# Optimization experiments

Measured on AMD Instinct MI355X. Metric: run time of the kernel, lower is better.

Reference implementation:

```python
import jax, jax.numpy as jnp
import numpy as np
import math

N, DIM = 131072, 128
NUM_CODEBOOKS, CODEBOOK_SIZE = 4, 2048
COMMIT_COST = 0.25


def setup_inputs() -> dict:
    key = jax.random.key(0)
    k1, k2 = jax.random.split(key)
    z_e = jax.random.normal(k1, (N, DIM), dtype=jnp.float32)
    codebooks = jax.random.normal(k2, (NUM_CODEBOOKS, CODEBOOK_SIZE, DIM), dtype=jnp.float32) / math.sqrt(DIM)
    return {"z_e": z_e, "codebooks": codebooks}


def _rvq(z_e, codebooks):
    # Sequential residual quantization stages via scan over codebooks.
    def stage(residual, codebook):
        x_norm = jnp.sum(residual * residual, axis=1, keepdims=True)
        c_norm = jnp.sum(codebook * codebook, axis=1)[None, :]
        d = x_norm - 2.0 * (residual @ codebook.T) + c_norm
        idx = jnp.argmin(d, axis=1)            # [N]
        q = codebook[idx]                      # [N, dim]
        return residual - q, (q, idx)

    _, (qs, idxs) = jax.lax.scan(stage, z_e, codebooks)
    quantized_sum = jnp.sum(qs, axis=0)        # [N, dim]
    codes = idxs.T                             # [N, num_codebooks]
    return quantized_sum, codes


def reference(z_e, codebooks):
    quantized_sum, codes = _rvq(z_e, codebooks)
    sg = jax.lax.stop_gradient
    codebook_loss = jnp.mean((sg(quantized_sum) - z_e) ** 2)
    commit_loss = jnp.mean((quantized_sum - sg(z_e)) ** 2)
    loss = codebook_loss + COMMIT_COST * commit_loss
    # straight-through estimator
    z_q = z_e + sg(quantized_sum - z_e)
    return (z_q, codes, loss)
```

## Files before the change

### kernel.cpp

```cpp
#include <hip/hip_runtime.h>

typedef float v16f __attribute__((ext_vector_type(16)));
typedef _Float16 v8h __attribute__((ext_vector_type(8)));

#define NROWS 131072
#define DIM 128
#define NCB 4
#define CBS 2048
#define ZQ_SIZE ((size_t)NROWS * DIM)
#define CODES_SIZE ((size_t)NROWS * NCB)
#define CHUNK_BYTES 16384
#define CBQ_TOTAL ((size_t)NCB * 64 * CHUNK_BYTES)
#define INV4096 2.44140625e-4f

#define MFMA16(a, b, c) __builtin_amdgcn_mfma_f32_32x32x16_f16((a), (b), (c), 0, 0, 0)

__global__ void prep_cb(const float* __restrict__ cb, _Float16* __restrict__ cbq) {
    const int g = blockIdx.x * 256 + threadIdx.x;
    const int c   = g & 7;
    const int col = (g >> 3) & 31;
    const int q   = (g >> 8) & 63;
    const int s   = g >> 14;
    const float* src = cb + (size_t)(s * CBS + q * 32 + col) * DIM + 16 * c;
    _Float16* base = cbq + (size_t)(s * 64 + q) * 8192;
#pragma unroll
    for (int hh = 0; hh < 2; ++hh) {
        v8h p0, p1;
#pragma unroll
        for (int j = 0; j < 8; ++j) {
            const float v = src[8 * hh + j];
            const _Float16 h0 = (_Float16)v;
            const float t = v - (float)h0;
            p0[j] = h0;
            p1[j] = (_Float16)(t * 4096.0f);
        }
        *reinterpret_cast<v8h*>(base + (size_t)c * 512 + (hh * 32 + col) * 8) = p0;
        *reinterpret_cast<v8h*>(base + (size_t)(8 + c) * 512 + (hh * 32 + col) * 8) = p1;
    }
}

__global__ void prep_cn(const float* __restrict__ cb, float* __restrict__ cn) {
    const int g = blockIdx.x * 256 + threadIdx.x;
    const float* src = cb + (size_t)g * DIM;
    float acc = 0.0f;
    for (int i = 0; i < 32; ++i) {
        const float4 v = *reinterpret_cast<const float4*>(src + 4 * i);
        acc = fmaf(v.x, v.x, acc); acc = fmaf(v.y, v.y, acc);
        acc = fmaf(v.z, v.z, acc); acc = fmaf(v.w, v.w, acc);
    }
    cn[g] = acc;
}

__global__ __launch_bounds__(256, 2)
void rvq_main(const float* __restrict__ ze, const float* __restrict__ cbf,
              const _Float16* __restrict__ cbq, const float* __restrict__ cn,
              float* __restrict__ out)
{
    __shared__ __align__(16) char BB[2][CHUNK_BYTES];
    __shared__ float XN[4][32];
    __shared__ int   BIs[4][32];

    const int tid  = threadIdx.x;
    const int wid  = tid >> 6;
    const int lane = tid & 63;
    const int col  = lane & 31;
    const int h    = lane >> 5;
    const int rowbase = blockIdx.x * 128 + wid * 32;
    const int myrow   = rowbase + col;

    float res[8][8];
#pragma unroll
    for (int c = 0; c < 8; ++c) {
#pragma unroll
        for (int w2 = 0; w2 < 2; ++w2) {
            const float4 v = *reinterpret_cast<const float4*>(
                ze + (size_t)myrow * DIM + 16 * c + 8 * h + 4 * w2);
            res[c][4 * w2 + 0] = v.x; res[c][4 * w2 + 1] = v.y;
            res[c][4 * w2 + 2] = v.z; res[c][4 * w2 + 3] = v.w;
        }
    }

    for (int s = 0; s < NCB; ++s) {
        v8h A0[8], A1[8];
        float pc[8];
#pragma unroll
        for (int c = 0; c < 8; ++c) {
            float p[8];
#pragma unroll
            for (int j = 0; j < 8; ++j) {
                const float v = res[c][j];
                p[j] = v * v;
                const _Float16 h0 = (_Float16)v;
                const float t = v - (float)h0;
                A0[c][j] = h0;
                A1[c][j] = (_Float16)(t * 4096.0f);
            }
            pc[c] = ((p[0] + p[1]) + (p[2] + p[3])) + ((p[4] + p[5]) + (p[6] + p[7]));
        }
        float xnp = ((pc[0] + pc[1]) + (pc[2] + pc[3])) + ((pc[4] + pc[5]) + (pc[6] + pc[7]));
        const float xn_own = xnp + __shfl_xor(xnp, 32);
        if (h == 0) XN[wid][col] = xn_own;
        __syncthreads();
        float xns[16];
#pragma unroll
        for (int r = 0; r < 16; ++r) xns[r] = XN[wid][(r & 3) + 8 * (r >> 2) + 4 * h];

        {
            const char* g0 = (const char*)cbq + (size_t)(s * 64) * CHUNK_BYTES;
#pragma unroll
            for (int i = 0; i < 4; ++i) {
                const int blk = i * 4 + wid;
                __builtin_amdgcn_global_load_lds(
                    (const __attribute__((address_space(1))) void*)(g0 + blk * 1024 + lane * 16),
                    (__attribute__((address_space(3))) void*)(&BB[0][blk * 1024]),
                    16, 0, 0);
            }
        }
        __syncthreads();

        float bestd[16]; int besti[16];
#pragma unroll
        for (int r = 0; r < 16; ++r) { bestd[r] = INFINITY; besti[r] = 0; }

#pragma unroll 1
        for (int q = 0; q < 64; ++q) {
            const int cur = q & 1;
            if (q < 63) {
                const char* gq = (const char*)cbq + (size_t)(s * 64 + q + 1) * CHUNK_BYTES;
#pragma unroll
                for (int i = 0; i < 4; ++i) {
                    const int blk = i * 4 + wid;
                    __builtin_amdgcn_global_load_lds(
                        (const __attribute__((address_space(1))) void*)(gq + blk * 1024 + lane * 16),
                        (__attribute__((address_space(3))) void*)(&BB[cur ^ 1][blk * 1024]),
                        16, 0, 0);
                }
            }
            const float cnv = cn[s * CBS + q * 32 + col];
            const char* bb = &BB[cur][0];
            v16f aM, aC;
            {
                const v8h b0 = *reinterpret_cast<const v8h*>(bb + lane * 16);
                const v8h b1 = *reinterpret_cast<const v8h*>(bb + 8 * 1024 + lane * 16);
                const v16f Z = {0.f,0.f,0.f,0.f,0.f,0.f,0.f,0.f,0.f,0.f,0.f,0.f,0.f,0.f,0.f,0.f};
                aM = MFMA16(A0[0], b0, Z);
                aC = MFMA16(A1[0], b0, Z);
                aC = MFMA16(A0[0], b1, aC);
            }
#pragma unroll
            for (int c = 1; c < 8; ++c) {
                const v8h b0 = *reinterpret_cast<const v8h*>(bb + (size_t)c * 1024 + lane * 16);
                const v8h b1 = *reinterpret_cast<const v8h*>(bb + (size_t)(8 + c) * 1024 + lane * 16);
                aM = MFMA16(A0[c], b0, aM);
                aC = MFMA16(A1[c], b0, aC);
                aC = MFMA16(A0[c], b1, aC);
            }
            const int code = q * 32 + col;
#pragma unroll
            for (int r = 0; r < 16; ++r) {
                const float dotf = fmaf(aC[r], INV4096, aM[r]);
                const float d = fmaf(-2.0f, dotf, xns[r]) + cnv;
                if (d < bestd[r]) { bestd[r] = d; besti[r] = code; }
            }
            __syncthreads();
        }

#pragma unroll
        for (int r = 0; r < 16; ++r) {
            float d = bestd[r]; int bi = besti[r];
#pragma unroll
            for (int m = 1; m <= 16; m <<= 1) {
                const float od = __shfl_xor(d, m);
                const int   oi = __shfl_xor(bi, m);
                const bool take = (od < d) || ((od == d) && (oi < bi));
                d  = take ? od : d;
                bi = take ? oi : bi;
            }
            bestd[r] = d; besti[r] = bi;
        }

        if (col == 0) {
#pragma unroll
            for (int r = 0; r < 16; ++r) {
                const int row16 = (r & 3) + 8 * (r >> 2) + 4 * h;
                BIs[wid][row16] = besti[r];
                out[ZQ_SIZE + (size_t)(rowbase + row16) * NCB + s] = (float)besti[r];
            }
        }
        __syncthreads();

        const int mybest = BIs[wid][col];
        const float* qrow = cbf + ((size_t)(s * CBS) + mybest) * DIM + 8 * h;
#pragma unroll
        for (int c = 0; c < 8; ++c) {
#pragma unroll
            for (int w2 = 0; w2 < 2; ++w2) {
                const float4 v = *reinterpret_cast<const float4*>(qrow + 16 * c + 4 * w2);
                res[c][4 * w2 + 0] -= v.x; res[c][4 * w2 + 1] -= v.y;
                res[c][4 * w2 + 2] -= v.z; res[c][4 * w2 + 3] -= v.w;
            }
        }
    }

    float lsum = 0.0f;
#pragma unroll
    for (int c = 0; c < 8; ++c) {
#pragma unroll
        for (int w2 = 0; w2 < 2; ++w2) {
            const float4 z = *reinterpret_cast<const float4*>(
                ze + (size_t)myrow * DIM + 16 * c + 8 * h + 4 * w2);
            const float r0 = res[c][4 * w2 + 0], r1 = res[c][4 * w2 + 1];
            const float r2 = res[c][4 * w2 + 2], r3 = res[c][4 * w2 + 3];
            float4 o;
            o.x = z.x - r0; o.y = z.y - r1; o.z = z.z - r2; o.w = z.w - r3;
            *reinterpret_cast<float4*>(out + (size_t)myrow * DIM + 16 * c + 8 * h + 4 * w2) = o;
            lsum = fmaf(r0, r0, lsum); lsum = fmaf(r1, r1, lsum);
            lsum = fmaf(r2, r2, lsum); lsum = fmaf(r3, r3, lsum);
        }
    }
#pragma unroll
    for (int m = 1; m < 64; m <<= 1) lsum += __shfl_xor(lsum, m);
    if (lane == 0)
        atomicAdd(out + ZQ_SIZE + CODES_SIZE, lsum * (1.25f / 16777216.0f));
}

extern "C" void kernel_launch(void* const* d_in, const int* in_sizes, int n_in,
                              void* d_out, int out_size, void* d_ws, size_t ws_size,
                              hipStream_t stream)
{
    const float* ze  = (const float*)d_in[0];
    const float* cbf = (const float*)d_in[1];
    float* out = (float*)d_out;

    _Float16* cbq = (_Float16*)d_ws;
    float* cnall = (float*)((char*)d_ws + CBQ_TOTAL);

    hipMemsetAsync(out + ZQ_SIZE + CODES_SIZE, 0, sizeof(float), stream);

    prep_cb<<<256, 256, 0, stream>>>(cbf, cbq);
    prep_cn<<<32, 256, 0, stream>>>(cbf, cnall);
    rvq_main<<<NROWS / 128, 256, 0, stream>>>(ze, cbf, cbq, cnall, out);
}
```

Baseline: 857.6 us.

## Recompute residual from history to cut registers, triple-buffer codebook chunks

Stops holding the 64-float residual in registers across stages. Each stage instead rebuilds it from z_e and the codebook rows selected so far. The argmin index is packed as 8-bit chunk ids, norm broadcast uses shuffles instead of LDS, and occupancy is raised to 3 blocks per CU. Codebook chunks are now triple-buffered with explicit vmcnt-based barriers so two chunks are in flight at once. The cost is extra global and cache reloads of z_e and codebook rows, and correctness depends on the hand-written waitcnt barriers.

```diff
diff --git a/kernel.cpp b/kernel.cpp
--- a/kernel.cpp
+++ b/kernel.cpp
@@ -51,14 +51,29 @@
     cn[g] = acc;
 }
 
-__global__ __launch_bounds__(256, 2)
+#define BAR_N4 do { \
+    __builtin_amdgcn_sched_barrier(0); \
+    asm volatile("s_waitcnt vmcnt(4) lgkmcnt(0)" ::: "memory"); \
+    __builtin_amdgcn_s_barrier(); \
+    asm volatile("" ::: "memory"); \
+    __builtin_amdgcn_sched_barrier(0); \
+} while (0)
+
+#define BAR_N0 do { \
+    __builtin_amdgcn_sched_barrier(0); \
+    asm volatile("s_waitcnt vmcnt(0) lgkmcnt(0)" ::: "memory"); \
+    __builtin_amdgcn_s_barrier(); \
+    asm volatile("" ::: "memory"); \
+    __builtin_amdgcn_sched_barrier(0); \
+} while (0)
+
+__global__ __launch_bounds__(256, 3)
 void rvq_main(const float* __restrict__ ze, const float* __restrict__ cbf,
               const _Float16* __restrict__ cbq, const float* __restrict__ cn,
               float* __restrict__ out)
 {
-    __shared__ __align__(16) char BB[2][CHUNK_BYTES];
-    __shared__ float XN[4][32];
-    __shared__ int   BIs[4][32];
+    __shared__ __align__(16) char BB[3][CHUNK_BYTES];
+    __shared__ int BIs[4][32];
 
     const int tid  = threadIdx.x;
     const int wid  = tid >> 6;
@@ -68,27 +83,35 @@
     const int rowbase = blockIdx.x * 128 + wid * 32;
     const int myrow   = rowbase + col;
 
-    float res[8][8];
-#pragma unroll
-    for (int c = 0; c < 8; ++c) {
-#pragma unroll
-        for (int w2 = 0; w2 < 2; ++w2) {
-            const float4 v = *reinterpret_cast<const float4*>(
-                ze + (size_t)myrow * DIM + 16 * c + 8 * h + 4 * w2);
-            res[c][4 * w2 + 0] = v.x; res[c][4 * w2 + 1] = v.y;
-            res[c][4 * w2 + 2] = v.z; res[c][4 * w2 + 3] = v.w;
-        }
-    }
-
+    const float* zrow = ze + (size_t)myrow * DIM + 8 * h;
+    int hist0 = 0, hist1 = 0, hist2 = 0, hist3 = 0;
+
+#pragma unroll
     for (int s = 0; s < NCB; ++s) {
         v8h A0[8], A1[8];
         float pc[8];
 #pragma unroll
         for (int c = 0; c < 8; ++c) {
+            float r8[8];
+            {
+                const float4 v0 = *reinterpret_cast<const float4*>(zrow + 16 * c);
+                const float4 v1 = *reinterpret_cast<const float4*>(zrow + 16 * c + 4);
+                r8[0] = v0.x; r8[1] = v0.y; r8[2] = v0.z; r8[3] = v0.w;
+                r8[4] = v1.x; r8[5] = v1.y; r8[6] = v1.z; r8[7] = v1.w;
+            }
+#pragma unroll
+            for (int t = 0; t < s; ++t) {
+                const int ht = (t == 0) ? hist0 : (t == 1) ? hist1 : (t == 2) ? hist2 : hist3;
+                const float* qrow = cbf + ((size_t)(t * CBS) + ht) * DIM + 16 * c + 8 * h;
+                const float4 q0 = *reinterpret_cast<const float4*>(qrow);
+                const float4 q1 = *reinterpret_cast<const float4*>(qrow + 4);
+                r8[0] -= q0.x; r8[1] -= q0.y; r8[2] -= q0.z; r8[3] -= q0.w;
+                r8[4] -= q1.x; r8[5] -= q1.y; r8[6] -= q1.z; r8[7] -= q1.w;
+            }
             float p[8];
 #pragma unroll
             for (int j = 0; j < 8; ++j) {
-                const float v = res[c][j];
+                const float v = r8[j];
                 p[j] = v * v;
                 const _Float16 h0 = (_Float16)v;
                 const float t = v - (float)h0;
@@ -97,46 +120,48 @@
             }
             pc[c] = ((p[0] + p[1]) + (p[2] + p[3])) + ((p[4] + p[5]) + (p[6] + p[7]));
         }
-        float xnp = ((pc[0] + pc[1]) + (pc[2] + pc[3])) + ((pc[4] + pc[5]) + (pc[6] + pc[7]));
+        const float xnp = ((pc[0] + pc[1]) + (pc[2] + pc[3])) + ((pc[4] + pc[5]) + (pc[6] + pc[7]));
         const float xn_own = xnp + __shfl_xor(xnp, 32);
-        if (h == 0) XN[wid][col] = xn_own;
-        __syncthreads();
         float xns[16];
 #pragma unroll
-        for (int r = 0; r < 16; ++r) xns[r] = XN[wid][(r & 3) + 8 * (r >> 2) + 4 * h];
-
-        {
-            const char* g0 = (const char*)cbq + (size_t)(s * 64) * CHUNK_BYTES;
+        for (int r = 0; r < 16; ++r)
+            xns[r] = __shfl(xn_own, (r & 3) + 8 * (r >> 2) + 4 * h);
+
+        const char* cbq_s = (const char*)cbq + (size_t)(s * 64) * CHUNK_BYTES;
+
+#pragma unroll
+        for (int qq = 0; qq < 2; ++qq) {
+            const char* gsrc = cbq_s + (size_t)qq * CHUNK_BYTES;
 #pragma unroll
             for (int i = 0; i < 4; ++i) {
                 const int blk = i * 4 + wid;
                 __builtin_amdgcn_global_load_lds(
-                    (const __attribute__((address_space(1))) void*)(g0 + blk * 1024 + lane * 16),
-                    (__attribute__((address_space(3))) void*)(&BB[0][blk * 1024]),
-                    16, 0, 0);
-            }
-        }
-        __syncthreads();
-
-        float bestd[16]; int besti[16];
-#pragma unroll
-        for (int r = 0; r < 16; ++r) { bestd[r] = INFINITY; besti[r] = 0; }
-
+                    (const __attribute__((address_space(1))) void*)(gsrc + blk * 1024 + lane * 16),
+                    (__attribute__((address_space(3))) void*)(&BB[qq][blk * 1024]), 16, 0, 0);
+            }
+        }
+        BAR_N4;
+
+        float bestd[16];
+        unsigned bq[4] = {0u, 0u, 0u, 0u};
+#pragma unroll
+        for (int r = 0; r < 16; ++r) bestd[r] = INFINITY;
+
+        int cur = 0;
 #pragma unroll 1
         for (int q = 0; q < 64; ++q) {
-            const int cur = q & 1;
-            if (q < 63) {
-                const char* gq = (const char*)cbq + (size_t)(s * 64 + q + 1) * CHUNK_BYTES;
+            const float cnv = cn[s * CBS + q * 32 + col];
+            if (q < 62) {
+                int pre = cur - 1; if (pre < 0) pre = 2;
+                const char* gsrc = cbq_s + (size_t)(q + 2) * CHUNK_BYTES;
 #pragma unroll
                 for (int i = 0; i < 4; ++i) {
                     const int blk = i * 4 + wid;
                     __builtin_amdgcn_global_load_lds(
-                        (const __attribute__((address_space(1))) void*)(gq + blk * 1024 + lane * 16),
-                        (__attribute__((address_space(3))) void*)(&BB[cur ^ 1][blk * 1024]),
-                        16, 0, 0);
+                        (const __attribute__((address_space(1))) void*)(gsrc + blk * 1024 + lane * 16),
+                        (__attribute__((address_space(3))) void*)(&BB[pre][blk * 1024]), 16, 0, 0);
                 }
             }
-            const float cnv = cn[s * CBS + q * 32 + col];
             const char* bb = &BB[cur][0];
             v16f aM, aC;
             {
@@ -155,16 +180,24 @@
                 aC = MFMA16(A1[c], b0, aC);
                 aC = MFMA16(A0[c], b1, aC);
             }
-            const int code = q * 32 + col;
 #pragma unroll
             for (int r = 0; r < 16; ++r) {
                 const float dotf = fmaf(aC[r], INV4096, aM[r]);
                 const float d = fmaf(-2.0f, dotf, xns[r]) + cnv;
-                if (d < bestd[r]) { bestd[r] = d; besti[r] = code; }
-            }
-            __syncthreads();
-        }
-
+                const bool take = d < bestd[r];
+                bestd[r] = take ? d : bestd[r];
+                const int w = r >> 2, sh = (r & 3) * 8;
+                const unsigned nb = (bq[w] & ~(255u << sh)) | ((unsigned)q << sh);
+                bq[w] = take ? nb : bq[w];
+            }
+            if (q < 62) { BAR_N4; } else { BAR_N0; }
+            cur = (cur == 2) ? 0 : cur + 1;
+        }
+
+        int besti[16];
+#pragma unroll
+        for (int r = 0; r < 16; ++r)
+            besti[r] = (int)((bq[r >> 2] >> ((r & 3) * 8)) & 255u) * 32 + col;
 #pragma unroll
         for (int r = 0; r < 16; ++r) {
             float d = bestd[r]; int bi = besti[r];
@@ -187,36 +220,43 @@
                 out[ZQ_SIZE + (size_t)(rowbase + row16) * NCB + s] = (float)besti[r];
             }
         }
-        __syncthreads();
-
+        asm volatile("s_waitcnt lgkmcnt(0)" ::: "memory");
         const int mybest = BIs[wid][col];
-        const float* qrow = cbf + ((size_t)(s * CBS) + mybest) * DIM + 8 * h;
-#pragma unroll
-        for (int c = 0; c < 8; ++c) {
-#pragma unroll
-            for (int w2 = 0; w2 < 2; ++w2) {
-                const float4 v = *reinterpret_cast<const float4*>(qrow + 16 * c + 4 * w2);
-                res[c][4 * w2 + 0] -= v.x; res[c][4 * w2 + 1] -= v.y;
-                res[c][4 * w2 + 2] -= v.z; res[c][4 * w2 + 3] -= v.w;
-            }
-        }
+        if (s == 0) hist0 = mybest;
+        else if (s == 1) hist1 = mybest;
+        else if (s == 2) hist2 = mybest;
+        else hist3 = mybest;
     }
 
     float lsum = 0.0f;
 #pragma unroll
     for (int c = 0; c < 8; ++c) {
-#pragma unroll
-        for (int w2 = 0; w2 < 2; ++w2) {
-            const float4 z = *reinterpret_cast<const float4*>(
-                ze + (size_t)myrow * DIM + 16 * c + 8 * h + 4 * w2);
-            const float r0 = res[c][4 * w2 + 0], r1 = res[c][4 * w2 + 1];
-            const float r2 = res[c][4 * w2 + 2], r3 = res[c][4 * w2 + 3];
-            float4 o;
-            o.x = z.x - r0; o.y = z.y - r1; o.z = z.z - r2; o.w = z.w - r3;
-            *reinterpret_cast<float4*>(out + (size_t)myrow * DIM + 16 * c + 8 * h + 4 * w2) = o;
-            lsum = fmaf(r0, r0, lsum); lsum = fmaf(r1, r1, lsum);
-            lsum = fmaf(r2, r2, lsum); lsum = fmaf(r3, r3, lsum);
-        }
+        float z8[8], r8[8];
+        {
+            const float4 v0 = *reinterpret_cast<const float4*>(zrow + 16 * c);
+            const float4 v1 = *reinterpret_cast<const float4*>(zrow + 16 * c + 4);
+            z8[0] = v0.x; z8[1] = v0.y; z8[2] = v0.z; z8[3] = v0.w;
+            z8[4] = v1.x; z8[5] = v1.y; z8[6] = v1.z; z8[7] = v1.w;
+        }
+#pragma unroll
+        for (int j = 0; j < 8; ++j) r8[j] = z8[j];
+#pragma unroll
+        for (int t = 0; t < 4; ++t) {
+            const int ht = (t == 0) ? hist0 : (t == 1) ? hist1 : (t == 2) ? hist2 : hist3;
+            const float* qrow = cbf + ((size_t)(t * CBS) + ht) * DIM + 16 * c + 8 * h;
+            const float4 q0 = *reinterpret_cast<const float4*>(qrow);
+            const float4 q1 = *reinterpret_cast<const float4*>(qrow + 4);
+            r8[0] -= q0.x; r8[1] -= q0.y; r8[2] -= q0.z; r8[3] -= q0.w;
+            r8[4] -= q1.x; r8[5] -= q1.y; r8[6] -= q1.z; r8[7] -= q1.w;
+        }
+        float4 o0, o1;
+        o0.x = z8[0] - r8[0]; o0.y = z8[1] - r8[1]; o0.z = z8[2] - r8[2]; o0.w = z8[3] - r8[3];
+        o1.x = z8[4] - r8[4]; o1.y = z8[5] - r8[5]; o1.z = z8[6] - r8[6]; o1.w = z8[7] - r8[7];
+        float* orow = out + (size_t)myrow * DIM + 16 * c + 8 * h;
+        *reinterpret_cast<float4*>(orow) = o0;
+        *reinterpret_cast<float4*>(orow + 4) = o1;
+#pragma unroll
+        for (int j = 0; j < 8; ++j) lsum = fmaf(r8[j], r8[j], lsum);
     }
 #pragma unroll
     for (int m = 1; m < 64; m <<= 1) lsum += __shfl_xor(lsum, m);
```

New measurement: 1.007 ms. 1.17x slower.

## Drop fp32 residual registers via fp16 triple split, raise occupancy to three blocks

Applied to the files above, without the earlier changes.

The fp32 residual array (64 registers per thread) is removed. The residual is instead stored as three fp16 pieces: two kept in registers as MFMA operands and the third spilled to scratch space in the output buffer. It is rebuilt from those pieces at each stage, which frees registers so launch bounds can rise to three blocks per CU. The change also replaces the LDS row-norm exchange and one barrier with wave shuffles, adds s_setprio around the MFMA block, and makes the argmin update branchless. The costs are extra global traffic for the scratch piece, the reconstruction arithmetic, and a slight change in residual precision.

```diff
diff --git a/kernel.cpp b/kernel.cpp
--- a/kernel.cpp
+++ b/kernel.cpp
@@ -51,14 +51,22 @@
     cn[g] = acc;
 }
 
-__global__ __launch_bounds__(256, 2)
+__device__ __forceinline__ void split3(float v, _Float16* h0, _Float16* h1, _Float16* h2) {
+    const _Float16 a = (_Float16)v;
+    const float t1 = v - (float)a;
+    const float s1 = t1 * 4096.0f;
+    const _Float16 b = (_Float16)s1;
+    const float s2 = (s1 - (float)b) * 4096.0f;
+    *h0 = a; *h1 = b; *h2 = (_Float16)s2;
+}
+
+__global__ __launch_bounds__(256, 3)
 void rvq_main(const float* __restrict__ ze, const float* __restrict__ cbf,
               const _Float16* __restrict__ cbq, const float* __restrict__ cn,
               float* __restrict__ out)
 {
     __shared__ __align__(16) char BB[2][CHUNK_BYTES];
-    __shared__ float XN[4][32];
-    __shared__ int   BIs[4][32];
+    __shared__ int BIs[4][32];
 
     const int tid  = threadIdx.x;
     const int wid  = tid >> 6;
@@ -68,53 +76,71 @@
     const int rowbase = blockIdx.x * 128 + wid * 32;
     const int myrow   = rowbase + col;
 
-    float res[8][8];
-#pragma unroll
-    for (int c = 0; c < 8; ++c) {
-#pragma unroll
-        for (int w2 = 0; w2 < 2; ++w2) {
-            const float4 v = *reinterpret_cast<const float4*>(
-                ze + (size_t)myrow * DIM + 16 * c + 8 * h + 4 * w2);
-            res[c][4 * w2 + 0] = v.x; res[c][4 * w2 + 1] = v.y;
-            res[c][4 * w2 + 2] = v.z; res[c][4 * w2 + 3] = v.w;
-        }
-    }
+    const float* zrow = ze + (size_t)myrow * DIM + 8 * h;
+    _Float16* a2 = (_Float16*)out + (size_t)blockIdx.x * 32768;
+
+    v8h A0[8], A1[8];
+    int mylast = 0;
 
     for (int s = 0; s < NCB; ++s) {
-        v8h A0[8], A1[8];
         float pc[8];
-#pragma unroll
-        for (int c = 0; c < 8; ++c) {
-            float p[8];
-#pragma unroll
-            for (int j = 0; j < 8; ++j) {
-                const float v = res[c][j];
-                p[j] = v * v;
-                const _Float16 h0 = (_Float16)v;
-                const float t = v - (float)h0;
-                A0[c][j] = h0;
-                A1[c][j] = (_Float16)(t * 4096.0f);
-            }
-            pc[c] = ((p[0] + p[1]) + (p[2] + p[3])) + ((p[4] + p[5]) + (p[6] + p[7]));
-        }
-        float xnp = ((pc[0] + pc[1]) + (pc[2] + pc[3])) + ((pc[4] + pc[5]) + (pc[6] + pc[7]));
+        if (s == 0) {
+#pragma unroll
+            for (int c = 0; c < 8; ++c) {
+                const float4 v0 = *reinterpret_cast<const float4*>(zrow + 16 * c);
+                const float4 v1 = *reinterpret_cast<const float4*>(zrow + 16 * c + 4);
+                float v[8] = {v0.x, v0.y, v0.z, v0.w, v1.x, v1.y, v1.z, v1.w};
+                v8h a2v;
+                float p[8];
+#pragma unroll
+                for (int j = 0; j < 8; ++j) {
+                    p[j] = v[j] * v[j];
+                    _Float16 x0, x1, x2;
+                    split3(v[j], &x0, &x1, &x2);
+                    A0[c][j] = x0; A1[c][j] = x1; a2v[j] = x2;
+                }
+                *reinterpret_cast<v8h*>(a2 + ((size_t)c * 256 + tid) * 8) = a2v;
+                pc[c] = ((p[0] + p[1]) + (p[2] + p[3])) + ((p[4] + p[5]) + (p[6] + p[7]));
+            }
+        } else {
+            const float* qrow = cbf + ((size_t)((s - 1) * CBS) + mylast) * DIM + 8 * h;
+#pragma unroll
+            for (int c = 0; c < 8; ++c) {
+                const v8h a2v_old = *reinterpret_cast<const v8h*>(a2 + ((size_t)c * 256 + tid) * 8);
+                const float4 q0 = *reinterpret_cast<const float4*>(qrow + 16 * c);
+                const float4 q1 = *reinterpret_cast<const float4*>(qrow + 16 * c + 4);
+                const float qv[8] = {q0.x, q0.y, q0.z, q0.w, q1.x, q1.y, q1.z, q1.w};
+                v8h a2v;
+                float p[8];
+#pragma unroll
+                for (int j = 0; j < 8; ++j) {
+                    const float vr = fmaf((float)a2v_old[j], 0x1p-24f,
+                                     fmaf((float)A1[c][j], 0x1p-12f, (float)A0[c][j]));
+                    const float v = vr - qv[j];
+                    p[j] = v * v;
+                    _Float16 x0, x1, x2;
+                    split3(v, &x0, &x1, &x2);
+                    A0[c][j] = x0; A1[c][j] = x1; a2v[j] = x2;
+                }
+                *reinterpret_cast<v8h*>(a2 + ((size_t)c * 256 + tid) * 8) = a2v;
+                pc[c] = ((p[0] + p[1]) + (p[2] + p[3])) + ((p[4] + p[5]) + (p[6] + p[7]));
+            }
+        }
+        const float xnp = ((pc[0] + pc[1]) + (pc[2] + pc[3])) + ((pc[4] + pc[5]) + (pc[6] + pc[7]));
         const float xn_own = xnp + __shfl_xor(xnp, 32);
-        if (h == 0) XN[wid][col] = xn_own;
-        __syncthreads();
         float xns[16];
 #pragma unroll
-        for (int r = 0; r < 16; ++r) xns[r] = XN[wid][(r & 3) + 8 * (r >> 2) + 4 * h];
-
-        {
-            const char* g0 = (const char*)cbq + (size_t)(s * 64) * CHUNK_BYTES;
-#pragma unroll
-            for (int i = 0; i < 4; ++i) {
-                const int blk = i * 4 + wid;
-                __builtin_amdgcn_global_load_lds(
-                    (const __attribute__((address_space(1))) void*)(g0 + blk * 1024 + lane * 16),
-                    (__attribute__((address_space(3))) void*)(&BB[0][blk * 1024]),
-                    16, 0, 0);
-            }
+        for (int r = 0; r < 16; ++r)
+            xns[r] = __shfl(xn_own, (r & 3) + 8 * (r >> 2) + 4 * h);
+
+        const char* cbq_s = (const char*)cbq + (size_t)(s * 64) * CHUNK_BYTES;
+
+#pragma unroll
+        for (int i = 0; i < 4; ++i) {
+            const int blk = i * 4 + wid;
+            __builtin_amdgcn_global_load_lds(
+                (const __attribute__((address_space(1))) void*)(cbq_s + blk * 1024 + lane * 16),
+                (__attribute__((address_space(3))) void*)(&BB[0][blk * 1024]), 16, 0, 0);
         }
         __syncthreads();
 
@@ -125,20 +151,20 @@
 #pragma unroll 1
         for (int q = 0; q < 64; ++q) {
             const int cur = q & 1;
+            const float cnv = cn[s * CBS + q * 32 + col];
             if (q < 63) {
-                const char* gq = (const char*)cbq + (size_t)(s * 64 + q + 1) * CHUNK_BYTES;
+                const char* gq = cbq_s + (size_t)(q + 1) * CHUNK_BYTES;
 #pragma unroll
                 for (int i = 0; i < 4; ++i) {
                     const int blk = i * 4 + wid;
                     __builtin_amdgcn_global_load_lds(
                         (const __attribute__((address_space(1))) void*)(gq + blk * 1024 + lane * 16),
-                        (__attribute__((address_space(3))) void*)(&BB[cur ^ 1][blk * 1024]),
-                        16, 0, 0);
+                        (__attribute__((address_space(3))) void*)(&BB[cur ^ 1][blk * 1024]), 16, 0, 0);
                 }
             }
-            const float cnv = cn[s * CBS + q * 32 + col];
             const char* bb = &BB[cur][0];
             v16f aM, aC;
+            __builtin_amdgcn_s_setprio(1);
             {
                 const v8h b0 = *reinterpret_cast<const v8h*>(bb + lane * 16);
                 const v8h b1 = *reinterpret_cast<const v8h*>(bb + 8 * 1024 + lane * 16);
@@ -155,12 +181,15 @@
                 aC = MFMA16(A1[c], b0, aC);
                 aC = MFMA16(A0[c], b1, aC);
             }
-            const int code = q * 32 + col;
+            __builtin_amdgcn_s_setprio(0);
+            const int code = (q << 5) | col;
 #pragma unroll
             for (int r = 0; r < 16; ++r) {
                 const float dotf = fmaf(aC[r], INV4096, aM[r]);
                 const float d = fmaf(-2.0f, dotf, xns[r]) + cnv;
-                if (d < bestd[r]) { bestd[r] = d; besti[r] = code; }
+                const bool take = d < bestd[r];
+                bestd[r] = take ? d : bestd[r];
+                besti[r] = take ? code : besti[r];
             }
             __syncthreads();
         }
@@ -188,35 +217,39 @@
             }
         }
         __syncthreads();
-
-        const int mybest = BIs[wid][col];
-        const float* qrow = cbf + ((size_t)(s * CBS) + mybest) * DIM + 8 * h;
-#pragma unroll
-        for (int c = 0; c < 8; ++c) {
-#pragma unroll
-            for (int w2 = 0; w2 < 2; ++w2) {
-                const float4 v = *reinterpret_cast<const float4*>(qrow + 16 * c + 4 * w2);
-                res[c][4 * w2 + 0] -= v.x; res[c][4 * w2 + 1] -= v.y;
-                res[c][4 * w2 + 2] -= v.z; res[c][4 * w2 + 3] -= v.w;
-            }
-        }
-    }
-
+        mylast = BIs[wid][col];
+    }
+
+    v8h a2r[8];
+#pragma unroll
+    for (int c = 0; c < 8; ++c)
+        a2r[c] = *reinterpret_cast<const v8h*>(a2 + ((size_t)c * 256 + tid) * 8);
+    __syncthreads();
+
+    const float* qrow = cbf + ((size_t)(3 * CBS) + mylast) * DIM + 8 * h;
     float lsum = 0.0f;
 #pragma unroll
     for (int c = 0; c < 8; ++c) {
-#pragma unroll
-        for (int w2 = 0; w2 < 2; ++w2) {
-            const float4 z = *reinterpret_cast<const float4*>(
-                ze + (size_t)myrow * DIM + 16 * c + 8 * h + 4 * w2);
-            const float r0 = res[c][4 * w2 + 0], r1 = res[c][4 * w2 + 1];
-            const float r2 = res[c][4 * w2 + 2], r3 = res[c][4 * w2 + 3];
-            float4 o;
-            o.x = z.x - r0; o.y = z.y - r1; o.z = z.z - r2; o.w = z.w - r3;
-            *reinterpret_cast<float4*>(out + (size_t)myrow * DIM + 16 * c + 8 * h + 4 * w2) = o;
-            lsum = fmaf(r0, r0, lsum); lsum = fmaf(r1, r1, lsum);
-            lsum = fmaf(r2, r2, lsum); lsum = fmaf(r3, r3, lsum);
-        }
+        const float4 q0 = *reinterpret_cast<const float4*>(qrow + 16 * c);
+        const float4 q1 = *reinterpret_cast<const float4*>(qrow + 16 * c + 4);
+        const float4 z0 = *reinterpret_cast<const float4*>(zrow + 16 * c);
+        const float4 z1 = *reinterpret_cast<const float4*>(zrow + 16 * c + 4);
+        const float qv[8] = {q0.x, q0.y, q0.z, q0.w, q1.x, q1.y, q1.z, q1.w};
+        const float zv[8] = {z0.x, z0.y, z0.z, z0.w, z1.x, z1.y, z1.z, z1.w};
+        float o[8];
+#pragma unroll
+        for (int j = 0; j < 8; ++j) {
+            const float vr = fmaf((float)a2r[c][j], 0x1p-24f,
+                             fmaf((float)A1[c][j], 0x1p-12f, (float)A0[c][j]));
+            const float v = vr - qv[j];
+            o[j] = zv[j] - v;
+            lsum = fmaf(v, v, lsum);
+        }
+        float4 o0 = {o[0], o[1], o[2], o[3]};
+        float4 o1 = {o[4], o[5], o[6], o[7]};
+        float* orow = out + (size_t)myrow * DIM + 16 * c + 8 * h;
+        *reinterpret_cast<float4*>(orow) = o0;
+        *reinterpret_cast<float4*>(orow + 4) = o1;
     }
 #pragma unroll
     for (int m = 1; m < 64; m <<= 1) lsum += __shfl_xor(lsum, m);
@@ -235,7 +268,7 @@
     _Float16* cbq = (_Float16*)d_ws;
     float* cnall = (float*)((char*)d_ws + CBQ_TOTAL);
 
-    hipMemsetAsync(out + ZQ_SIZE + CODES_SIZE, 0, sizeof(float), stream);
+    (void)hipMemsetAsync(out + ZQ_SIZE + CODES_SIZE, 0, sizeof(float), stream);
 
     prep_cb<<<256, 256, 0, stream>>>(cbf, cbq);
     prep_cn<<<32, 256, 0, stream>>>(cbf, cnall);
```

Measured after the change: 960.9 us. +12.0%, slower.

## Process two codebook chunks per barrier and pack best indices into bytes

Applied to the files above, without the earlier changes.

The main loop now loads 32KB periods (two 32-code chunks) per double-buffer step, which halves the number of block-wide barriers per stage. The first period's load is issued before the residual fp16 split so it overlaps that work. The row norm is broadcast with shuffles instead of going through shared memory. Best-code indices are stored as 8-bit chunk ids packed four per register to save registers, and s_setprio raises wave priority around the MFMA block. The cost is doubled LDS usage (64KB per block), which may limit the two-blocks-per-CU occupancy target.

```diff
diff --git a/kernel.cpp b/kernel.cpp
--- a/kernel.cpp
+++ b/kernel.cpp
@@ -1,6 +1,7 @@
 #include <hip/hip_runtime.h>
 
 typedef float v16f __attribute__((ext_vector_type(16)));
+typedef float v4f __attribute__((ext_vector_type(4)));
 typedef _Float16 v8h __attribute__((ext_vector_type(8)));
 
 #define NROWS 131072
@@ -10,6 +11,7 @@
 #define ZQ_SIZE ((size_t)NROWS * DIM)
 #define CODES_SIZE ((size_t)NROWS * NCB)
 #define CHUNK_BYTES 16384
+#define PERIOD_BYTES 32768
 #define CBQ_TOTAL ((size_t)NCB * 64 * CHUNK_BYTES)
 #define INV4096 2.44140625e-4f
 
@@ -44,7 +46,7 @@
     const float* src = cb + (size_t)g * DIM;
     float acc = 0.0f;
     for (int i = 0; i < 32; ++i) {
-        const float4 v = *reinterpret_cast<const float4*>(src + 4 * i);
+        const v4f v = *reinterpret_cast<const v4f*>(src + 4 * i);
         acc = fmaf(v.x, v.x, acc); acc = fmaf(v.y, v.y, acc);
         acc = fmaf(v.z, v.z, acc); acc = fmaf(v.w, v.w, acc);
     }
@@ -56,9 +58,8 @@
               const _Float16* __restrict__ cbq, const float* __restrict__ cn,
               float* __restrict__ out)
 {
-    __shared__ __align__(16) char BB[2][CHUNK_BYTES];
-    __shared__ float XN[4][32];
-    __shared__ int   BIs[4][32];
+    __shared__ __align__(16) char BB[2][PERIOD_BYTES];
+    __shared__ int BIs[4][32];
 
     const int tid  = threadIdx.x;
     const int wid  = tid >> 6;
@@ -68,19 +69,31 @@
     const int rowbase = blockIdx.x * 128 + wid * 32;
     const int myrow   = rowbase + col;
 
+    const float* zrow = ze + (size_t)myrow * DIM + 8 * h;
+
     float res[8][8];
 #pragma unroll
     for (int c = 0; c < 8; ++c) {
 #pragma unroll
         for (int w2 = 0; w2 < 2; ++w2) {
-            const float4 v = *reinterpret_cast<const float4*>(
-                ze + (size_t)myrow * DIM + 16 * c + 8 * h + 4 * w2);
+            const v4f v = *reinterpret_cast<const v4f*>(zrow + 16 * c + 4 * w2);
             res[c][4 * w2 + 0] = v.x; res[c][4 * w2 + 1] = v.y;
             res[c][4 * w2 + 2] = v.z; res[c][4 * w2 + 3] = v.w;
         }
     }
 
+#pragma unroll 1
     for (int s = 0; s < NCB; ++s) {
+        const char* cbq_s = (const char*)cbq + (size_t)(s * 64) * CHUNK_BYTES;
+
+#pragma unroll
+        for (int u = 0; u < 8; ++u) {
+            const int off = (u * 4 + wid) * 1024 + lane * 16;
+            __builtin_amdgcn_global_load_lds(
+                (const __attribute__((address_space(1))) void*)(cbq_s + off),
+                (__attribute__((address_space(3))) void*)(&BB[0][off]), 16, 0, 0);
+        }
+
         v8h A0[8], A1[8];
         float pc[8];
 #pragma unroll
@@ -97,77 +110,77 @@
             }
             pc[c] = ((p[0] + p[1]) + (p[2] + p[3])) + ((p[4] + p[5]) + (p[6] + p[7]));
         }
-        float xnp = ((pc[0] + pc[1]) + (pc[2] + pc[3])) + ((pc[4] + pc[5]) + (pc[6] + pc[7]));
+        const float xnp = ((pc[0] + pc[1]) + (pc[2] + pc[3])) + ((pc[4] + pc[5]) + (pc[6] + pc[7]));
         const float xn_own = xnp + __shfl_xor(xnp, 32);
-        if (h == 0) XN[wid][col] = xn_own;
+        float xns[16];
+#pragma unroll
+        for (int r = 0; r < 16; ++r)
+            xns[r] = __shfl(xn_own, (r & 3) + 8 * (r >> 2) + 4 * h);
+
+        float bestd[16];
+        unsigned bq[4] = {0u, 0u, 0u, 0u};
+#pragma unroll
+        for (int r = 0; r < 16; ++r) bestd[r] = INFINITY;
+
         __syncthreads();
-        float xns[16];
-#pragma unroll
-        for (int r = 0; r < 16; ++r) xns[r] = XN[wid][(r & 3) + 8 * (r >> 2) + 4 * h];
-
-        {
-            const char* g0 = (const char*)cbq + (size_t)(s * 64) * CHUNK_BYTES;
-#pragma unroll
-            for (int i = 0; i < 4; ++i) {
-                const int blk = i * 4 + wid;
-                __builtin_amdgcn_global_load_lds(
-                    (const __attribute__((address_space(1))) void*)(g0 + blk * 1024 + lane * 16),
-                    (__attribute__((address_space(3))) void*)(&BB[0][blk * 1024]),
-                    16, 0, 0);
-            }
-        }
-        __syncthreads();
-
-        float bestd[16]; int besti[16];
-#pragma unroll
-        for (int r = 0; r < 16; ++r) { bestd[r] = INFINITY; besti[r] = 0; }
 
 #pragma unroll 1
-        for (int q = 0; q < 64; ++q) {
-            const int cur = q & 1;
-            if (q < 63) {
-                const char* gq = (const char*)cbq + (size_t)(s * 64 + q + 1) * CHUNK_BYTES;
-#pragma unroll
-                for (int i = 0; i < 4; ++i) {
-                    const int blk = i * 4 + wid;
+        for (int p = 0; p < 32; ++p) {
+            const int cur = p & 1;
+            const float cnv0 = cn[s * CBS + (2 * p) * 32 + col];
+            const float cnv1 = cn[s * CBS + (2 * p + 1) * 32 + col];
+            if (p < 31) {
+                const char* gp = cbq_s + (size_t)(p + 1) * PERIOD_BYTES;
+#pragma unroll
+                for (int u = 0; u < 8; ++u) {
+                    const int off = (u * 4 + wid) * 1024 + lane * 16;
                     __builtin_amdgcn_global_load_lds(
-                        (const __attribute__((address_space(1))) void*)(gq + blk * 1024 + lane * 16),
-                        (__attribute__((address_space(3))) void*)(&BB[cur ^ 1][blk * 1024]),
-                        16, 0, 0);
-                }
-            }
-            const float cnv = cn[s * CBS + q * 32 + col];
-            const char* bb = &BB[cur][0];
-            v16f aM, aC;
-            {
-                const v8h b0 = *reinterpret_cast<const v8h*>(bb + lane * 16);
-                const v8h b1 = *reinterpret_cast<const v8h*>(bb + 8 * 1024 + lane * 16);
-                const v16f Z = {0.f,0.f,0.f,0.f,0.f,0.f,0.f,0.f,0.f,0.f,0.f,0.f,0.f,0.f,0.f,0.f};
-                aM = MFMA16(A0[0], b0, Z);
-                aC = MFMA16(A1[0], b0, Z);
-                aC = MFMA16(A0[0], b1, aC);
-            }
-#pragma unroll
-            for (int c = 1; c < 8; ++c) {
-                const v8h b0 = *reinterpret_cast<const v8h*>(bb + (size_t)c * 1024 + lane * 16);
-                const v8h b1 = *reinterpret_cast<const v8h*>(bb + (size_t)(8 + c) * 1024 + lane * 16);
-                aM = MFMA16(A0[c], b0, aM);
-                aC = MFMA16(A1[c], b0, aC);
-                aC = MFMA16(A0[c], b1, aC);
-            }
-            const int code = q * 32 + col;
-#pragma unroll
-            for (int r = 0; r < 16; ++r) {
-                const float dotf = fmaf(aC[r], INV4096, aM[r]);
-                const float d = fmaf(-2.0f, dotf, xns[r]) + cnv;
-                if (d < bestd[r]) { bestd[r] = d; besti[r] = code; }
+                        (const __attribute__((address_space(1))) void*)(gp + off),
+                        (__attribute__((address_space(3))) void*)(&BB[cur ^ 1][off]), 16, 0, 0);
+                }
+            }
+#pragma unroll
+            for (int sc = 0; sc < 2; ++sc) {
+                const char* bb = &BB[cur][sc * CHUNK_BYTES];
+                const float cnv = sc ? cnv1 : cnv0;
+                const unsigned qg = (unsigned)(2 * p + sc);
+                v16f aM, aC;
+                __builtin_amdgcn_s_setprio(1);
+                {
+                    const v8h b0 = *reinterpret_cast<const v8h*>(bb + lane * 16);
+                    const v8h b1 = *reinterpret_cast<const v8h*>(bb + 8 * 1024 + lane * 16);
+                    const v16f Z = {0.f,0.f,0.f,0.f,0.f,0.f,0.f,0.f,0.f,0.f,0.f,0.f,0.f,0.f,0.f,0.f};
+                    aM = MFMA16(A0[0], b0, Z);
+                    aC = MFMA16(A1[0], b0, Z);
+                    aC = MFMA16(A0[0], b1, aC);
+                }
+#pragma unroll
+                for (int c = 1; c < 8; ++c) {
+                    const v8h b0 = *reinterpret_cast<const v8h*>(bb + (size_t)c * 1024 + lane * 16);
+                    const v8h b1 = *reinterpret_cast<const v8h*>(bb + (size_t)(8 + c) * 1024 + lane * 16);
+                    aM = MFMA16(A0[c], b0, aM);
+                    aC = MFMA16(A1[c], b0, aC);
+                    aC = MFMA16(A0[c], b1, aC);
+                }
+                __builtin_amdgcn_s_setprio(0);
+#pragma unroll
+                for (int r = 0; r < 16; ++r) {
+                    const int w = r >> 2, sh = (r & 3) * 8;
+                    const float dotf = fmaf(aC[r], INV4096, aM[r]);
+                    const float d = fmaf(-2.0f, dotf, xns[r]) + cnv;
+                    const bool take = d < bestd[r];
+                    bestd[r] = take ? d : bestd[r];
+                    const unsigned nb = (bq[w] & ~(255u << sh)) | (qg << sh);
+                    bq[w] = take ? nb : bq[w];
+                }
             }
             __syncthreads();
         }
 
 #pragma unroll
         for (int r = 0; r < 16; ++r) {
-            float d = bestd[r]; int bi = besti[r];
+            float d = bestd[r];
+            int bi = (int)((bq[r >> 2] >> ((r & 3) * 8)) & 255u) * 32 + col;
 #pragma unroll
             for (int m = 1; m <= 16; m <<= 1) {
                 const float od = __shfl_xor(d, m);
@@ -176,26 +189,21 @@
                 d  = take ? od : d;
                 bi = take ? oi : bi;
             }
-            bestd[r] = d; besti[r] = bi;
-        }
-
-        if (col == 0) {
-#pragma unroll
-            for (int r = 0; r < 16; ++r) {
+            if (col == 0) {
                 const int row16 = (r & 3) + 8 * (r >> 2) + 4 * h;
-                BIs[wid][row16] = besti[r];
-                out[ZQ_SIZE + (size_t)(rowbase + row16) * NCB + s] = (float)besti[r];
+                BIs[wid][row16] = bi;
+                out[ZQ_SIZE + (size_t)(rowbase + row16) * NCB + s] = (float)bi;
             }
         }
         __syncthreads();
-
         const int mybest = BIs[wid][col];
+
         const float* qrow = cbf + ((size_t)(s * CBS) + mybest) * DIM + 8 * h;
 #pragma unroll
         for (int c = 0; c < 8; ++c) {
 #pragma unroll
             for (int w2 = 0; w2 < 2; ++w2) {
-                const float4 v = *reinterpret_cast<const float4*>(qrow + 16 * c + 4 * w2);
+                const v4f v = *reinterpret_cast<const v4f*>(qrow + 16 * c + 4 * w2);
                 res[c][4 * w2 + 0] -= v.x; res[c][4 * w2 + 1] -= v.y;
                 res[c][4 * w2 + 2] -= v.z; res[c][4 * w2 + 3] -= v.w;
             }
@@ -207,13 +215,12 @@
     for (int c = 0; c < 8; ++c) {
 #pragma unroll
         for (int w2 = 0; w2 < 2; ++w2) {
-            const float4 z = *reinterpret_cast<const float4*>(
-                ze + (size_t)myrow * DIM + 16 * c + 8 * h + 4 * w2);
+            const v4f z = *reinterpret_cast<const v4f*>(zrow + 16 * c + 4 * w2);
             const float r0 = res[c][4 * w2 + 0], r1 = res[c][4 * w2 + 1];
             const float r2 = res[c][4 * w2 + 2], r3 = res[c][4 * w2 + 3];
-            float4 o;
+            v4f o;
             o.x = z.x - r0; o.y = z.y - r1; o.z = z.z - r2; o.w = z.w - r3;
-            *reinterpret_cast<float4*>(out + (size_t)myrow * DIM + 16 * c + 8 * h + 4 * w2) = o;
+            *reinterpret_cast<v4f*>(out + (size_t)myrow * DIM + 16 * c + 8 * h + 4 * w2) = o;
             lsum = fmaf(r0, r0, lsum); lsum = fmaf(r1, r1, lsum);
             lsum = fmaf(r2, r2, lsum); lsum = fmaf(r3, r3, lsum);
         }
@@ -235,7 +242,7 @@
     _Float16* cbq = (_Float16*)d_ws;
     float* cnall = (float*)((char*)d_ws + CBQ_TOTAL);
 
-    hipMemsetAsync(out + ZQ_SIZE + CODES_SIZE, 0, sizeof(float), stream);
+    (void)hipMemsetAsync(out + ZQ_SIZE + CODES_SIZE, 0, sizeof(float), stream);
 
     prep_cb<<<256, 256, 0, stream>>>(cbf, cbq);
     prep_cn<<<32, 256, 0, stream>>>(cbf, cnall);
```

Result: slower. 879.2 us (+2.5%).
